# Performance work log

Hardware: AMD Instinct MI355X
Metric: run time of the kernel (lower is better)

The kernel has to match this reference:

```python
import jax, jax.numpy as jnp
import numpy as np

HIDDEN = 1024
NUM_BLOCKS = 8
BLOCK = HIDDEN // NUM_BLOCKS  # 128
EPS = 1e-6


def cayley_batch(A):
    # A: [b, r, r] -> orthogonal Q = (I - S) @ inv(I + S + eps*I), S = 0.5*(A - A^T)
    b, r, _ = A.shape
    I = jnp.eye(r, dtype=A.dtype)
    S = 0.5 * (A - jnp.swapaxes(A, -2, -1))
    return jnp.matmul(I - S, jnp.linalg.inv(I + S + EPS * I))


def apply_block_diag(W, R):
    # W @ block_diag(R_0..R_{n-1}) without materializing the hidden x hidden matrix.
    # W: [out, hidden], R: [n, bs, bs]
    out = W.shape[0]
    Wb = W.reshape(out, NUM_BLOCKS, BLOCK)
    return jnp.einsum('onb,nbc->onc', Wb, R).reshape(out, NUM_BLOCKS * BLOCK)


def setup_inputs() -> dict:
    key = jax.random.key(0)
    ks = jax.random.split(key, 6)
    return {
        'attn_weight': jax.random.normal(ks[0], (3 * HIDDEN, HIDDEN), dtype=jnp.float32) * 0.02,
        'bias': jax.random.normal(ks[1], (3 * HIDDEN,), dtype=jnp.float32) * 0.02,
        'x': jax.random.normal(ks[2], (8, 4096, HIDDEN), dtype=jnp.float32),
        'q_R': jax.random.normal(ks[3], (NUM_BLOCKS, BLOCK, BLOCK), dtype=jnp.float32),
        'k_R': jax.random.normal(ks[4], (NUM_BLOCKS, BLOCK, BLOCK), dtype=jnp.float32),
        'v_R': jax.random.normal(ks[5], (NUM_BLOCKS, BLOCK, BLOCK), dtype=jnp.float32),
    }


def reference(attn_weight, bias, x, q_R, k_R, v_R):
    orth_q = cayley_batch(q_R)
    orth_k = cayley_batch(k_R)
    orth_v = cayley_batch(v_R)
    q_w, k_w, v_w = jnp.split(attn_weight, 3, axis=0)  # each [hidden, hidden]
    filt_q = apply_block_diag(q_w, orth_q)
    filt_k = apply_block_diag(k_w, orth_k)
    filt_v = apply_block_diag(v_w, orth_v)
    filt = jnp.concatenate([filt_q, filt_k, filt_v], axis=0)  # [3*hidden, hidden]
    # F.linear: x @ filt^T + bias -> [B, S, 3*hidden]
    return jnp.einsum('bsh,oh->bso', x, filt) + bias
```

## Files before the change

kernel.cpp:

```cpp
#include <hip/hip_runtime.h>

typedef __bf16 bf16x8 __attribute__((ext_vector_type(8)));
typedef float  f32x4  __attribute__((ext_vector_type(4)));

#define EPSC 1e-6f

__device__ __forceinline__ unsigned short f2bf(float f) {
  union { float f; unsigned int u; } c; c.f = f;
  unsigned int u = c.u;
  u = u + 0x7FFFu + ((u >> 16) & 1u);
  return (unsigned short)(u >> 16);
}
__device__ __forceinline__ float bf2f(unsigned short h) {
  union { unsigned int u; float f; } c; c.u = ((unsigned int)h) << 16;
  return c.f;
}
__device__ __forceinline__ void gl_lds16(const unsigned short* g, unsigned short* l) {
  __builtin_amdgcn_global_load_lds((const __attribute__((address_space(1))) void*)g,
                                   (__attribute__((address_space(3))) void*)l, 16, 0, 0);
}

__global__ void __launch_bounds__(256) cayley_k(const float* __restrict__ qR,
                                               const float* __restrict__ kR,
                                               const float* __restrict__ vR,
                                               float* __restrict__ wsL,
                                               float* __restrict__ wsQt) {
  extern __shared__ float A_s[];
  float4* A4 = (float4*)A_s;
  const int m = blockIdx.x;
  const float* R = (m < 8 ? qR : (m < 16 ? kR : vR)) + (size_t)(m & 7) * 16384;
  float* Lg = wsL  + (size_t)m * 16384;
  float* Qt = wsQt + (size_t)m * 16384;
  const int tid = threadIdx.x;

  for (int idx = tid; idx < 16384; idx += 256) {
    int i = idx >> 7, j = idx & 127;
    float s = 0.5f * (R[idx] - R[j * 128 + i]);
    float v = ((i == j) ? (1.0f + EPSC) : 0.0f) - s;
    A_s[idx] = v;
    Lg[idx] = v;
  }
  __syncthreads();

  const int c = tid & 31;
  const int rg = tid >> 5;
  for (int k = 0; k < 128; ++k) {
    __syncthreads();
    if (tid < 32) {
      float ip = 1.0f / A_s[k * 128 + k];
      float4 v = A4[k * 32 + tid];
      v.x *= ip; v.y *= ip; v.z *= ip; v.w *= ip;
      if (tid == (k >> 2)) {
        int k3 = k & 3;
        if (k3 == 0) v.x = ip; else if (k3 == 1) v.y = ip;
        else if (k3 == 2) v.z = ip; else v.w = ip;
      }
      A4[k * 32 + tid] = v;
    }
    __syncthreads();
    float4 rk = A4[k * 32 + c];
    const int kc = k >> 2, k3 = k & 3;
    float ipv = (k3 == 0) ? rk.x : (k3 == 1) ? rk.y : (k3 == 2) ? rk.z : rk.w;
#pragma unroll
    for (int pass = 0; pass < 16; ++pass) {
      int i = pass * 8 + rg;
      if (i != k) {
        float mi = A_s[i * 128 + k];
        float4 v = A4[i * 32 + c];
        v.x -= mi * rk.x; v.y -= mi * rk.y; v.z -= mi * rk.z; v.w -= mi * rk.w;
        if (c == kc) {
          float fx = -mi * ipv;
          if (k3 == 0) v.x = fx; else if (k3 == 1) v.y = fx;
          else if (k3 == 2) v.z = fx; else v.w = fx;
        }
        A4[i * 32 + c] = v;
      }
    }
  }
  __syncthreads();

  const int ti = tid >> 4, tj = tid & 15;
  const int i0 = ti * 8, j0 = tj * 8;
  float acc[8][8];
#pragma unroll
  for (int r = 0; r < 8; ++r)
#pragma unroll
    for (int s = 0; s < 8; ++s) acc[r][s] = 0.f;

  for (int tc = 0; tc < 32; ++tc) {
    float4 b4[8];
#pragma unroll
    for (int s = 0; s < 8; ++s)
      b4[s] = *(const float4*)&Lg[(size_t)(j0 + s) * 128 + tc * 4];
#pragma unroll
    for (int r = 0; r < 8; ++r) {
      float4 a4 = A4[(i0 + r) * 32 + tc];
#pragma unroll
      for (int s = 0; s < 8; ++s)
        acc[r][s] += a4.x * b4[s].x + a4.y * b4[s].y + a4.z * b4[s].z + a4.w * b4[s].w;
    }
  }
#pragma unroll
  for (int r = 0; r < 8; ++r)
#pragma unroll
    for (int s = 0; s < 8; ++s) {
      float v = acc[r][s] - EPSC * A_s[(i0 + r) * 128 + j0 + s];
      Qt[(size_t)(i0 + r) * 128 + j0 + s] = v;
    }
}

__global__ void __launch_bounds__(256) filt_k(const float* __restrict__ W,
                                              const float* __restrict__ wsQt,
                                              unsigned short* __restrict__ filt) {
  __shared__ unsigned short Qs[128 * 136];
  const int m = blockIdx.x;
  const int ot = blockIdx.y;
  const int mset = m >> 3, n = m & 7;
  const float* Qt = wsQt + (size_t)m * 16384;
  const int tid = threadIdx.x;

  for (int idx = tid; idx < 16384; idx += 256) {
    int i = idx >> 7, j = idx & 127;
    Qs[i * 136 + j] = f2bf(Qt[idx]);
  }
  __syncthreads();

  const int ol = tid & 63, cg = tid >> 6;
  const int go = mset * 1024 + ot * 64 + ol;
  const float* Wrow = W + (size_t)go * 1024 + n * 128;

  float acc[32];
#pragma unroll
  for (int i = 0; i < 32; ++i) acc[i] = 0.f;

  for (int b4 = 0; b4 < 32; ++b4) {
    float4 w4 = *(const float4*)(Wrow + b4 * 4);
#pragma unroll
    for (int cc = 0; cc < 32; ++cc) {
      int cidx = cg * 32 + cc;
      ushort4 q4 = *(const ushort4*)&Qs[cidx * 136 + b4 * 4];
      acc[cc] += w4.x * bf2f(q4.x) + w4.y * bf2f(q4.y)
               + w4.z * bf2f(q4.z) + w4.w * bf2f(q4.w);
    }
  }
  unsigned short* dst = filt + (size_t)go * 1024 + n * 128 + cg * 32;
#pragma unroll
  for (int g2 = 0; g2 < 8; ++g2) {
    ushort4 o;
    o.x = f2bf(acc[g2 * 4 + 0]); o.y = f2bf(acc[g2 * 4 + 1]);
    o.z = f2bf(acc[g2 * 4 + 2]); o.w = f2bf(acc[g2 * 4 + 3]);
    *(ushort4*)(dst + g2 * 4) = o;
  }
}

__global__ void __launch_bounds__(256) cvt_k(const float4* __restrict__ in,
                                             ushort4* __restrict__ out, int n4) {
  int i = blockIdx.x * 256 + threadIdx.x;
  int stride = gridDim.x * 256;
  for (; i < n4; i += stride) {
    float4 v = in[i];
    ushort4 o;
    o.x = f2bf(v.x); o.y = f2bf(v.y); o.z = f2bf(v.z); o.w = f2bf(v.w);
    out[i] = o;
  }
}

__global__ void __launch_bounds__(256) gemm_k(const unsigned short* __restrict__ Ax,
                                              const unsigned short* __restrict__ Bf,
                                              const float* __restrict__ bias,
                                              float* __restrict__ C) {
  __shared__ unsigned short As[128 * 32];
  __shared__ unsigned short Bs[128 * 32];
  const int tid = threadIdx.x;
  const int bx = blockIdx.x;
  const int by = blockIdx.y;
  const int lane = tid & 63, wave = tid >> 6;
  const int wm = wave & 1, wn = wave >> 1;
  const int quad = lane >> 4, l16 = lane & 15;
  const long mbase = (long)by * 128;
  const long nbase = (long)bx * 128;

  f32x4 acc[4][4];
#pragma unroll
  for (int i = 0; i < 4; ++i)
#pragma unroll
    for (int j = 0; j < 4; ++j) {
      acc[i][j][0] = 0.f; acc[i][j][1] = 0.f; acc[i][j][2] = 0.f; acc[i][j][3] = 0.f;
    }

  const int q0 = tid, q1 = 256 + tid;
  const int row0 = q0 >> 2, c0 = (q0 & 3) * 8;
  const int row1 = q1 >> 2, c1 = (q1 & 3) * 8;
  const unsigned short* a0 = Ax + (mbase + row0) * 1024 + c0;
  const unsigned short* a1 = Ax + (mbase + row1) * 1024 + c1;
  const unsigned short* b0 = Bf + (nbase + row0) * 1024 + c0;
  const unsigned short* b1 = Bf + (nbase + row1) * 1024 + c1;
  unsigned short* lA0 = &As[q0 * 8]; unsigned short* lA1 = &As[q1 * 8];
  unsigned short* lB0 = &Bs[q0 * 8]; unsigned short* lB1 = &Bs[q1 * 8];

  for (int kk = 0; kk < 1024; kk += 32) {
    gl_lds16(a0 + kk, lA0);
    gl_lds16(a1 + kk, lA1);
    gl_lds16(b0 + kk, lB0);
    gl_lds16(b1 + kk, lB1);
    __syncthreads();

    bf16x8 af[4], bf[4];
#pragma unroll
    for (int mi = 0; mi < 4; ++mi)
      af[mi] = *(const bf16x8*)&As[(wm * 64 + mi * 16 + l16) * 32 + quad * 8];
#pragma unroll
    for (int ni = 0; ni < 4; ++ni)
      bf[ni] = *(const bf16x8*)&Bs[(wn * 64 + ni * 16 + l16) * 32 + quad * 8];
#pragma unroll
    for (int mi = 0; mi < 4; ++mi)
#pragma unroll
      for (int ni = 0; ni < 4; ++ni)
        acc[mi][ni] = __builtin_amdgcn_mfma_f32_16x16x32_bf16(af[mi], bf[ni], acc[mi][ni], 0, 0, 0);
    __syncthreads();
  }

#pragma unroll
  for (int ni = 0; ni < 4; ++ni) {
    long gcol = nbase + wn * 64 + ni * 16 + l16;
    float bv = bias[gcol];
#pragma unroll
    for (int mi = 0; mi < 4; ++mi) {
      long grow = mbase + wm * 64 + mi * 16 + quad * 4;
#pragma unroll
      for (int r = 0; r < 4; ++r)
        C[(grow + r) * 3072 + gcol] = acc[mi][ni][r] + bv;
    }
  }
}

extern "C" void kernel_launch(void* const* d_in, const int* in_sizes, int n_in,
                              void* d_out, int out_size, void* d_ws, size_t ws_size,
                              hipStream_t stream) {
  const float* W    = (const float*)d_in[0];
  const float* bias = (const float*)d_in[1];
  const float* x    = (const float*)d_in[2];
  const float* qR   = (const float*)d_in[3];
  const float* kR   = (const float*)d_in[4];
  const float* vR   = (const float*)d_in[5];
  float* out = (float*)d_out;

  char* ws = (char*)d_ws;
  float* wsL           = (float*)(ws);
  float* wsQt          = (float*)(ws + 1572864);
  unsigned short* wsF  = (unsigned short*)(ws + 3145728);
  unsigned short* wsX  = (unsigned short*)(ws + 9437184);

  cayley_k<<<24, 256, 65536, stream>>>(qR, kR, vR, wsL, wsQt);
  filt_k<<<dim3(24, 16), 256, 0, stream>>>(W, wsQt, wsF);
  cvt_k<<<4096, 256, 0, stream>>>((const float4*)x, (ushort4*)wsX, 33554432 / 4);
  gemm_k<<<dim3(24, 256), 256, 0, stream>>>(wsX, wsF, bias, out);
}
```

Measured before the change: 1.052 ms.

## Fuse Cayley inversion with x conversion into one launch and widen Cayley blocks

Merges the x fp32→bf16 conversion kernel into the Cayley kernel as extra blocks, so the 24 serial Gauss-Jordan blocks run alongside the bandwidth-bound conversion instead of before it. The Cayley blocks grow to 512 threads: the elimination loop now batches its row loads across 8 rows per thread, and the final multiply gives each thread 4 rows. The cost is that every conversion block also reserves 64KB of dynamic LDS, which may limit how many blocks fit per CU. The pivot row is now written back unchanged while other threads read it, which is a benign race on identical values.

```diff
diff --git a/kernel.cpp b/kernel.cpp
--- a/kernel.cpp
+++ b/kernel.cpp
@@ -20,27 +20,42 @@
                                    (__attribute__((address_space(3))) void*)l, 16, 0, 0);
 }
 
-__global__ void __launch_bounds__(256) cayley_k(const float* __restrict__ qR,
-                                               const float* __restrict__ kR,
-                                               const float* __restrict__ vR,
-                                               float* __restrict__ wsL,
-                                               float* __restrict__ wsQt) {
+__global__ void __launch_bounds__(512) cayley_cvt_k(const float* __restrict__ qR,
+                                                    const float* __restrict__ kR,
+                                                    const float* __restrict__ vR,
+                                                    float* __restrict__ wsL,
+                                                    float* __restrict__ wsQt,
+                                                    const float4* __restrict__ xin,
+                                                    ushort4* __restrict__ xbf,
+                                                    int n4) {
   extern __shared__ float A_s[];
+  const int tid = threadIdx.x;
+
+  if (blockIdx.x >= 24) {
+    int i = (blockIdx.x - 24) * 512 + tid;
+    int stride = (gridDim.x - 24) * 512;
+    for (; i < n4; i += stride) {
+      float4 v = xin[i];
+      ushort4 o;
+      o.x = f2bf(v.x); o.y = f2bf(v.y); o.z = f2bf(v.z); o.w = f2bf(v.w);
+      xbf[i] = o;
+    }
+    return;
+  }
+
   float4* A4 = (float4*)A_s;
   const int m = blockIdx.x;
   const float* R = (m < 8 ? qR : (m < 16 ? kR : vR)) + (size_t)(m & 7) * 16384;
   float* Lg = wsL  + (size_t)m * 16384;
   float* Qt = wsQt + (size_t)m * 16384;
-  const int tid = threadIdx.x;
-
-  for (int idx = tid; idx < 16384; idx += 256) {
+
+  for (int idx = tid; idx < 16384; idx += 512) {
     int i = idx >> 7, j = idx & 127;
     float s = 0.5f * (R[idx] - R[j * 128 + i]);
     float v = ((i == j) ? (1.0f + EPSC) : 0.0f) - s;
     A_s[idx] = v;
     Lg[idx] = v;
   }
-  __syncthreads();
 
   const int c = tid & 31;
   const int rg = tid >> 5;
@@ -58,32 +73,39 @@
       A4[k * 32 + tid] = v;
     }
     __syncthreads();
+
     float4 rk = A4[k * 32 + c];
     const int kc = k >> 2, k3 = k & 3;
-    float ipv = (k3 == 0) ? rk.x : (k3 == 1) ? rk.y : (k3 == 2) ? rk.z : rk.w;
-#pragma unroll
-    for (int pass = 0; pass < 16; ++pass) {
-      int i = pass * 8 + rg;
-      if (i != k) {
-        float mi = A_s[i * 128 + k];
-        float4 v = A4[i * 32 + c];
-        v.x -= mi * rk.x; v.y -= mi * rk.y; v.z -= mi * rk.z; v.w -= mi * rk.w;
-        if (c == kc) {
-          float fx = -mi * ipv;
-          if (k3 == 0) v.x = fx; else if (k3 == 1) v.y = fx;
-          else if (k3 == 2) v.z = fx; else v.w = fx;
-        }
-        A4[i * 32 + c] = v;
+    const float ipv = (k3 == 0) ? rk.x : (k3 == 1) ? rk.y : (k3 == 2) ? rk.z : rk.w;
+
+    float mi[8];
+    float4 v[8];
+#pragma unroll
+    for (int p = 0; p < 8; ++p) mi[p] = A_s[(p * 16 + rg) * 128 + k];
+#pragma unroll
+    for (int p = 0; p < 8; ++p) v[p] = A4[(p * 16 + rg) * 32 + c];
+#pragma unroll
+    for (int p = 0; p < 8; ++p) {
+      const int i = p * 16 + rg;
+      const bool isk = (i == k);
+      const float mm = isk ? 0.0f : mi[p];
+      float4 w = v[p];
+      w.x -= mm * rk.x; w.y -= mm * rk.y; w.z -= mm * rk.z; w.w -= mm * rk.w;
+      if (c == kc && !isk) {
+        const float fx = -mm * ipv;
+        if (k3 == 0) w.x = fx; else if (k3 == 1) w.y = fx;
+        else if (k3 == 2) w.z = fx; else w.w = fx;
       }
+      A4[i * 32 + c] = w;
     }
   }
   __syncthreads();
 
   const int ti = tid >> 4, tj = tid & 15;
-  const int i0 = ti * 8, j0 = tj * 8;
-  float acc[8][8];
-#pragma unroll
-  for (int r = 0; r < 8; ++r)
+  const int i0 = ti * 4, j0 = tj * 8;
+  float acc[4][8];
+#pragma unroll
+  for (int r = 0; r < 4; ++r)
 #pragma unroll
     for (int s = 0; s < 8; ++s) acc[r][s] = 0.f;
 
@@ -93,7 +115,7 @@
     for (int s = 0; s < 8; ++s)
       b4[s] = *(const float4*)&Lg[(size_t)(j0 + s) * 128 + tc * 4];
 #pragma unroll
-    for (int r = 0; r < 8; ++r) {
+    for (int r = 0; r < 4; ++r) {
       float4 a4 = A4[(i0 + r) * 32 + tc];
 #pragma unroll
       for (int s = 0; s < 8; ++s)
@@ -101,7 +123,7 @@
     }
   }
 #pragma unroll
-  for (int r = 0; r < 8; ++r)
+  for (int r = 0; r < 4; ++r)
 #pragma unroll
     for (int s = 0; s < 8; ++s) {
       float v = acc[r][s] - EPSC * A_s[(i0 + r) * 128 + j0 + s];
@@ -150,18 +172,6 @@
     o.x = f2bf(acc[g2 * 4 + 0]); o.y = f2bf(acc[g2 * 4 + 1]);
     o.z = f2bf(acc[g2 * 4 + 2]); o.w = f2bf(acc[g2 * 4 + 3]);
     *(ushort4*)(dst + g2 * 4) = o;
-  }
-}
-
-__global__ void __launch_bounds__(256) cvt_k(const float4* __restrict__ in,
-                                             ushort4* __restrict__ out, int n4) {
-  int i = blockIdx.x * 256 + threadIdx.x;
-  int stride = gridDim.x * 256;
-  for (; i < n4; i += stride) {
-    float4 v = in[i];
-    ushort4 o;
-    o.x = f2bf(v.x); o.y = f2bf(v.y); o.z = f2bf(v.z); o.w = f2bf(v.w);
-    out[i] = o;
   }
 }
 
@@ -205,18 +215,18 @@
     gl_lds16(b1 + kk, lB1);
     __syncthreads();
 
-    bf16x8 af[4], bf[4];
+    bf16x8 af[4], bff[4];
 #pragma unroll
     for (int mi = 0; mi < 4; ++mi)
       af[mi] = *(const bf16x8*)&As[(wm * 64 + mi * 16 + l16) * 32 + quad * 8];
 #pragma unroll
     for (int ni = 0; ni < 4; ++ni)
-      bf[ni] = *(const bf16x8*)&Bs[(wn * 64 + ni * 16 + l16) * 32 + quad * 8];
+      bff[ni] = *(const bf16x8*)&Bs[(wn * 64 + ni * 16 + l16) * 32 + quad * 8];
 #pragma unroll
     for (int mi = 0; mi < 4; ++mi)
 #pragma unroll
       for (int ni = 0; ni < 4; ++ni)
-        acc[mi][ni] = __builtin_amdgcn_mfma_f32_16x16x32_bf16(af[mi], bf[ni], acc[mi][ni], 0, 0, 0);
+        acc[mi][ni] = __builtin_amdgcn_mfma_f32_16x16x32_bf16(af[mi], bff[ni], acc[mi][ni], 0, 0, 0);
     __syncthreads();
   }
 
@@ -251,8 +261,9 @@
   unsigned short* wsF  = (unsigned short*)(ws + 3145728);
   unsigned short* wsX  = (unsigned short*)(ws + 9437184);
 
-  cayley_k<<<24, 256, 65536, stream>>>(qR, kR, vR, wsL, wsQt);
+  cayley_cvt_k<<<24 + 2048, 512, 65536, stream>>>(qR, kR, vR, wsL, wsQt,
+                                                  (const float4*)x, (ushort4*)wsX,
+                                                  33554432 / 4);
   filt_k<<<dim3(24, 16), 256, 0, stream>>>(W, wsQt, wsF);
-  cvt_k<<<4096, 256, 0, stream>>>((const float4*)x, (ushort4*)wsX, 33554432 / 4);
   gemm_k<<<dim3(24, 256), 256, 0, stream>>>(wsX, wsF, bias, out);
 }
```

After: 913.5 us. 13.2% less time.
